# Kernel optimization log

Hardware: AMD Instinct MI355X
Metric: run time of the kernel (lower is better)

Reference implementation:

```python
import jax, jax.numpy as jnp
import numpy as np

T = 2048          # num tokens (prefill)
H = 4096          # hidden_size
NH = 32           # num query heads
NKV = 8           # num kv heads (GQA)
HD = H // NH      # head_dim = 128
BASE = 1000000.0  # rope_theta
NEG = -1e30


def _rope(x, positions):
    # NeoX-style rotary embedding (vLLM default). x: [T, nh, HD]
    half = HD // 2
    inv_freq = 1.0 / (BASE ** (jnp.arange(half, dtype=jnp.float32) / half))
    freqs = positions.astype(jnp.float32)[:, None] * inv_freq  # [T, half]
    cos = jnp.concatenate([jnp.cos(freqs), jnp.cos(freqs)], -1)[:, None, :]
    sin = jnp.concatenate([jnp.sin(freqs), jnp.sin(freqs)], -1)[:, None, :]
    rot = jnp.concatenate([-x[..., half:], x[..., :half]], -1)
    return x * cos + rot * sin


def setup_inputs() -> dict:
    key = jax.random.key(0)
    k1, k2, k3 = jax.random.split(key, 3)
    hidden_states = jax.random.normal(k1, (T, H), jnp.float32)
    wqkv = jax.random.normal(k2, (H, (NH + 2 * NKV) * HD), jnp.float32) * 0.02
    wo = jax.random.normal(k3, (NH * HD, H), jnp.float32) * 0.02
    positions = jnp.arange(T, dtype=jnp.int32)
    return {"positions": positions, "hidden_states": hidden_states,
            "wqkv": wqkv, "wo": wo}


def reference(positions, hidden_states, wqkv, wo):
    # fused QKV projection
    qkv = hidden_states @ wqkv                      # [T, (NH+2*NKV)*HD]
    q, k, v = jnp.split(qkv, [NH * HD, NH * HD + NKV * HD], axis=-1)
    q = q.reshape(T, NH, HD)
    k = k.reshape(T, NKV, HD)
    v = v.reshape(T, NKV, HD)
    # inline RoPE on q, k
    q = _rope(q, positions)
    k = _rope(k, positions)
    # GQA: expand kv heads to query heads
    rep = NH // NKV
    k = jnp.repeat(k, rep, axis=1)                  # [T, NH, HD]
    v = jnp.repeat(v, rep, axis=1)
    # causal scaled dot-product attention (prefill path of PagedAttention)
    scores = jnp.einsum('qhd,khd->hqk', q, k) * (HD ** -0.5)  # [NH, T, T]
    causal = positions[:, None] >= positions[None, :]          # [T, T]
    scores = jnp.where(causal[None, :, :], scores, NEG)
    probs = jax.nn.softmax(scores, axis=-1)
    attn = jnp.einsum('hqk,khd->qhd', probs, v).reshape(T, NH * HD)
    return attn @ wo
```

## Files before the change

### kernel.cpp

```cpp
#include <hip/hip_runtime.h>
#include <hip/hip_bf16.h>

typedef __attribute__((ext_vector_type(8))) short bf16x8;
typedef __attribute__((ext_vector_type(4))) float f32x4;
typedef unsigned short u16;

#define T_TOK 2048
#define HID 4096
#define NH 32
#define NKV 8
#define HD 128
#define QKVN 6144
#define KOFF 4096
#define VOFF 5120

static __device__ __forceinline__ float bf2f(u16 x) {
    union { float f; unsigned u; } v; v.u = ((unsigned)x) << 16; return v.f;
}
static __device__ __forceinline__ u16 f2bf(float f) {
    union { float f; unsigned u; } v; v.f = f;
    unsigned u = v.u;
    unsigned r = (u + 0x7fff + ((u >> 16) & 1)) >> 16;
    return (u16)r;
}

static __device__ __forceinline__ void gload16(const u16* g, u16* l) {
    __builtin_amdgcn_global_load_lds((const __attribute__((address_space(1))) void*)g,
                                     (__attribute__((address_space(3))) void*)l, 16, 0, 0);
}

__global__ __launch_bounds__(256) void convk(const float* __restrict__ in, u16* __restrict__ out) {
    int i = blockIdx.x * 256 + threadIdx.x;
    float4 v = ((const float4*)in)[i];
    ushort4 o;
    o.x = f2bf(v.x); o.y = f2bf(v.y); o.z = f2bf(v.z); o.w = f2bf(v.w);
    ((ushort4*)out)[i] = o;
}

__global__ __launch_bounds__(256) void transpk(const float* __restrict__ in, u16* __restrict__ out,
                                               int R, int C) {
    __shared__ float tile[64][65];
    int c0 = blockIdx.x * 64, r0 = blockIdx.y * 64;
    int tid = threadIdx.x;
#pragma unroll
    for (int it = 0; it < 4; ++it) {
        int ci = it * 256 + tid;
        int r = ci >> 4, c4 = (ci & 15) * 4;
        float4 v = *(const float4*)&in[(size_t)(r0 + r) * C + c0 + c4];
        tile[r][c4 + 0] = v.x; tile[r][c4 + 1] = v.y; tile[r][c4 + 2] = v.z; tile[r][c4 + 3] = v.w;
    }
    __syncthreads();
#pragma unroll
    for (int it = 0; it < 4; ++it) {
        int ci = it * 256 + tid;
        int c = ci >> 4, rq = (ci & 15) * 4;
        ushort4 o;
        o.x = f2bf(tile[rq + 0][c]); o.y = f2bf(tile[rq + 1][c]);
        o.z = f2bf(tile[rq + 2][c]); o.w = f2bf(tile[rq + 3][c]);
        *(ushort4*)&out[(size_t)(c0 + c) * R + r0 + rq] = o;
    }
}

template <int BN, int OUTF32>
__global__ __launch_bounds__(512) void gemm8p(const u16* __restrict__ A, const u16* __restrict__ Bt,
                                              void* __restrict__ Cout, int M, int N, int K) {
    constexpr int BM = 256, BK = 32;
    constexpr int WN = BN / 4;
    constexpr int NF = WN / 16;
    constexpr int ACALLS = 2;
    constexpr int BCALLS = BN / 128;
    constexpr int CALLS = ACALLS + BCALLS;
    constexpr int C1 = 2;
    constexpr int ABUF = BM * BK;
    constexpr int BBUF = BN * BK;
    constexpr int BUFSZ = ABUF + BBUF;

    __shared__ __attribute__((aligned(16))) u16 lds[4 * BUFSZ];

    int bid = blockIdx.x;
    int m0 = (bid & 7) * BM, n0 = (bid >> 3) * BN;
    int tid = threadIdx.x, lane = tid & 63, wid = tid >> 6;
    int wm = wid >> 2, wn = wid & 3;
    int l15 = lane & 15, g4 = lane >> 4;
    int srow = lane >> 2;
    int sslot = (lane & 3) ^ ((lane >> 3) & 3);
    int swz = (g4 ^ ((l15 >> 1) & 3)) * 8;
    int NK = K / BK;

    auto STAGE = [&](int kt, int c) {
        u16* base = &lds[(kt & 3) * BUFSZ];
        size_t kcol = (size_t)kt * BK + sslot * 8;
        if (c < ACALLS) {
            int ch = wid * ACALLS + c;
            gload16(&A[(size_t)(m0 + ch * 16 + srow) * K + kcol], base + ch * 512);
        } else {
            int ch = wid * BCALLS + (c - ACALLS);
            gload16(&Bt[(size_t)(n0 + ch * 16 + srow) * K + kcol], base + ABUF + ch * 512);
        }
    };

    f32x4 acc[8][NF];
#pragma unroll
    for (int i = 0; i < 8; ++i)
#pragma unroll
        for (int j = 0; j < NF; ++j) acc[i][j] = (f32x4){0.f, 0.f, 0.f, 0.f};

    for (int t = 0; t < 3; ++t)
        for (int c = 0; c < CALLS; ++c) STAGE(t, c);
    asm volatile("s_waitcnt vmcnt(%0)" :: "i"(2 * CALLS) : "memory");
    __builtin_amdgcn_s_barrier();
    __builtin_amdgcn_sched_barrier(0);

    for (int g = 0; g < NK; ++g) {
        const u16* ab = &lds[(g & 3) * BUFSZ];
        const u16* bb = ab + ABUF;

        bf16x8 bfr[NF], af[4];
#pragma unroll
        for (int j = 0; j < NF; ++j)
            bfr[j] = *(const bf16x8*)&bb[(wn * WN + j * 16 + l15) * BK + swz];
#pragma unroll
        for (int i = 0; i < 4; ++i)
            af[i] = *(const bf16x8*)&ab[(wm * 128 + i * 16 + l15) * BK + swz];
        if (g + 3 < NK) {
#pragma unroll
            for (int c = 0; c < C1; ++c) STAGE(g + 3, c);
        }
        __builtin_amdgcn_s_setprio(1);
#pragma unroll
        for (int i = 0; i < 4; ++i)
#pragma unroll
            for (int j = 0; j < NF; ++j)
                acc[i][j] = __builtin_amdgcn_mfma_f32_16x16x32_bf16(af[i], bfr[j], acc[i][j], 0, 0, 0);
        __builtin_amdgcn_s_setprio(0);

        bf16x8 af2[4];
#pragma unroll
        for (int i = 0; i < 4; ++i)
            af2[i] = *(const bf16x8*)&ab[(wm * 128 + (4 + i) * 16 + l15) * BK + swz];
        if (g + 3 < NK) {
#pragma unroll
            for (int c = C1; c < CALLS; ++c) STAGE(g + 3, c);
        }
        __builtin_amdgcn_s_setprio(1);
#pragma unroll
        for (int i = 0; i < 4; ++i)
#pragma unroll
            for (int j = 0; j < NF; ++j)
                acc[4 + i][j] = __builtin_amdgcn_mfma_f32_16x16x32_bf16(af2[i], bfr[j], acc[4 + i][j], 0, 0, 0);
        __builtin_amdgcn_s_setprio(0);

        if (g < NK - 3)       asm volatile("s_waitcnt vmcnt(%0)" :: "i"(2 * CALLS) : "memory");
        else if (g == NK - 3) asm volatile("s_waitcnt vmcnt(%0)" :: "i"(CALLS) : "memory");
        else if (g == NK - 2) asm volatile("s_waitcnt vmcnt(0)" ::: "memory");
        __builtin_amdgcn_s_barrier();
        __builtin_amdgcn_sched_barrier(0);
    }

#pragma unroll
    for (int mi = 0; mi < 8; ++mi)
#pragma unroll
        for (int j = 0; j < NF; ++j)
#pragma unroll
            for (int i = 0; i < 4; ++i) {
                int row = m0 + wm * 128 + mi * 16 + g4 * 4 + i;
                int col = n0 + wn * WN + j * 16 + l15;
                float v = acc[mi][j][i];
                if (OUTF32) ((float*)Cout)[(size_t)row * N + col] = v;
                else        ((u16*)Cout)[(size_t)row * N + col] = f2bf(v);
            }
}

__global__ __launch_bounds__(256) void ropek(u16* __restrict__ qkvb, const int* __restrict__ positions) {
    __shared__ float cs_[64], sn_[64];
    int t = blockIdx.x;
    float pos = (float)positions[t];
    if (threadIdx.x < 64) {
        int d = threadIdx.x;
        float inv = exp2f(-(float)d * (19.931568569324174f / 64.0f));
        float fr = pos * inv;
        cs_[d] = cosf(fr);
        sn_[d] = sinf(fr);
    }
    __syncthreads();
#pragma unroll
    for (int it = 0; it < 10; ++it) {
        int ci = it * 256 + threadIdx.x;
        int hh = ci >> 6, d = ci & 63;
        int base = (hh < NH) ? hh * HD : KOFF + (hh - NH) * HD;
        size_t off = (size_t)t * QKVN + base + d;
        float x1 = bf2f(qkvb[off]);
        float x2 = bf2f(qkvb[off + 64]);
        float s = sn_[d], c = cs_[d];
        qkvb[off]      = f2bf(x1 * c - x2 * s);
        qkvb[off + 64] = f2bf(x2 * c + x1 * s);
    }
}

__global__ __launch_bounds__(256) void vtranspk(const u16* __restrict__ qkvb, u16* __restrict__ vT) {
    __shared__ __attribute__((aligned(16))) u16 tile[64][136];
    int kvh = blockIdx.x, t0 = blockIdx.y * 64;
    int tid = threadIdx.x;
#pragma unroll
    for (int it = 0; it < 4; ++it) {
        int ci = it * 256 + tid;
        int r = ci >> 4, c8 = (ci & 15) * 8;
        *(bf16x8*)&tile[r][c8] = *(const bf16x8*)&qkvb[(size_t)(t0 + r) * QKVN + VOFF + kvh * HD + c8];
    }
    __syncthreads();
#pragma unroll
    for (int it = 0; it < 4; ++it) {
        int ci = it * 256 + tid;
        int d = ci >> 3, tc = (ci & 7) * 8;
        union { bf16x8 v; u16 u[8]; } o;
#pragma unroll
        for (int e = 0; e < 8; ++e) o.u[e] = tile[tc + e][d];
        *(bf16x8*)&vT[((size_t)kvh * HD + d) * T_TOK + t0 + tc] = o.v;
    }
}

__global__ __launch_bounds__(256) void attnk(const u16* __restrict__ qkvb, const u16* __restrict__ vT,
                                             u16* __restrict__ attnb) {
    __shared__ __attribute__((aligned(16))) u16 kt_[64 * 136];
    __shared__ __attribute__((aligned(16))) u16 vt_[128 * 72];
    __shared__ __attribute__((aligned(16))) u16 pl_[4 * 16 * 72];
    int h = blockIdx.x, qt = 31 - blockIdx.y;
    int kvh = h >> 2;
    int q0 = qt * 64;
    int tid = threadIdx.x, lane = tid & 63, wid = tid >> 6;
    int l15 = lane & 15, g = lane >> 4;
    const float scale = 0.08838834764831845f;

    int kr = tid >> 4, kc = (tid & 15) * 8;
    int vd = tid >> 3, vc = (tid & 7) * 8;
    const u16* kbase = qkvb + KOFF + (size_t)kvh * HD + kc;
    const u16* vbase = vT + ((size_t)kvh * HD) * T_TOK + vc;

    bf16x8 qf[4];
    int qrow = q0 + wid * 16 + l15;
#pragma unroll
    for (int ks = 0; ks < 4; ++ks)
        qf[ks] = *(const bf16x8*)&qkvb[(size_t)qrow * QKVN + h * HD + ks * 32 + g * 8];

    f32x4 o[8];
#pragma unroll
    for (int df = 0; df < 8; ++df) o[df] = (f32x4){0.f, 0.f, 0.f, 0.f};
    float m_run[4], l_run[4];
#pragma unroll
    for (int i = 0; i < 4; ++i) { m_run[i] = -3.0e38f; l_run[i] = 0.f; }

    bf16x8 kreg[4], vreg[4];
#pragma unroll
    for (int it = 0; it < 4; ++it)
        kreg[it] = *(const bf16x8*)&kbase[(size_t)(it * 16 + kr) * QKVN];
#pragma unroll
    for (int it = 0; it < 4; ++it)
        vreg[it] = *(const bf16x8*)&vbase[(size_t)(it * 32 + vd) * T_TOK];
#pragma unroll
    for (int it = 0; it < 4; ++it) *(bf16x8*)&kt_[(it * 16 + kr) * 136 + kc] = kreg[it];
#pragma unroll
    for (int it = 0; it < 4; ++it) *(bf16x8*)&vt_[(it * 32 + vd) * 72 + vc] = vreg[it];
    {
        int ktl = (1 <= qt) ? 1 : qt;
#pragma unroll
        for (int it = 0; it < 4; ++it)
            kreg[it] = *(const bf16x8*)&kbase[(size_t)(ktl * 64 + it * 16 + kr) * QKVN];
#pragma unroll
        for (int it = 0; it < 4; ++it)
            vreg[it] = *(const bf16x8*)&vbase[(size_t)(it * 32 + vd) * T_TOK + ktl * 64];
    }
    __syncthreads();

    for (int kt2 = 0; kt2 <= qt; ++kt2) {
        int kvb = kt2 * 64;

        f32x4 s[4];
#pragma unroll
        for (int nf = 0; nf < 4; ++nf) s[nf] = (f32x4){0.f, 0.f, 0.f, 0.f};
        __builtin_amdgcn_s_setprio(1);
#pragma unroll
        for (int ks = 0; ks < 4; ++ks) {
#pragma unroll
            for (int nf = 0; nf < 4; ++nf) {
                bf16x8 bfr = *(const bf16x8*)&kt_[(nf * 16 + l15) * 136 + ks * 32 + g * 8];
                s[nf] = __builtin_amdgcn_mfma_f32_16x16x32_bf16(qf[ks], bfr, s[nf], 0, 0, 0);
            }
        }
        __builtin_amdgcn_s_setprio(0);

        float mrow[4];
#pragma unroll
        for (int i = 0; i < 4; ++i) {
            int qr = q0 + wid * 16 + g * 4 + i;
            float mx = -3.0e38f;
#pragma unroll
            for (int nf = 0; nf < 4; ++nf) {
                int kvc = kvb + nf * 16 + l15;
                float v = s[nf][i] * scale;
                v = (kvc <= qr) ? v : -1.0e30f;
                s[nf][i] = v;
                mx = fmaxf(mx, v);
            }
            mrow[i] = mx;
        }
#pragma unroll
        for (int dd = 1; dd < 16; dd <<= 1)
#pragma unroll
            for (int i = 0; i < 4; ++i) mrow[i] = fmaxf(mrow[i], __shfl_xor(mrow[i], dd));

        int ok = 1;
#pragma unroll
        for (int i = 0; i < 4; ++i) ok &= (mrow[i] <= m_run[i] + 8.0f) ? 1 : 0;
        if (!__all(ok)) {
            float alpha[4];
#pragma unroll
            for (int i = 0; i < 4; ++i) {
                float mnew = fmaxf(m_run[i], mrow[i]);
                alpha[i] = __expf(m_run[i] - mnew);
                m_run[i] = mnew;
                l_run[i] *= alpha[i];
            }
#pragma unroll
            for (int df = 0; df < 8; ++df)
#pragma unroll
                for (int i = 0; i < 4; ++i) o[df][i] *= alpha[i];
        }

        float rsum[4] = {0.f, 0.f, 0.f, 0.f};
#pragma unroll
        for (int nf = 0; nf < 4; ++nf)
#pragma unroll
            for (int i = 0; i < 4; ++i) {
                float p = __expf(s[nf][i] - m_run[i]);
                rsum[i] += p;
                pl_[wid * 1152 + (g * 4 + i) * 72 + nf * 16 + l15] = f2bf(p);
            }
#pragma unroll
        for (int dd = 1; dd < 16; dd <<= 1)
#pragma unroll
            for (int i = 0; i < 4; ++i) rsum[i] += __shfl_xor(rsum[i], dd);
#pragma unroll
        for (int i = 0; i < 4; ++i) l_run[i] += rsum[i];

        __builtin_amdgcn_s_setprio(1);
#pragma unroll
        for (int ks2 = 0; ks2 < 2; ++ks2) {
            bf16x8 af = *(const bf16x8*)&pl_[wid * 1152 + l15 * 72 + ks2 * 32 + g * 8];
#pragma unroll
            for (int df = 0; df < 8; ++df) {
                bf16x8 bfr = *(const bf16x8*)&vt_[(df * 16 + l15) * 72 + ks2 * 32 + g * 8];
                o[df] = __builtin_amdgcn_mfma_f32_16x16x32_bf16(af, bfr, o[df], 0, 0, 0);
            }
        }
        __builtin_amdgcn_s_setprio(0);

        if (kt2 < qt) {
            __syncthreads();
#pragma unroll
            for (int it = 0; it < 4; ++it) *(bf16x8*)&kt_[(it * 16 + kr) * 136 + kc] = kreg[it];
#pragma unroll
            for (int it = 0; it < 4; ++it) *(bf16x8*)&vt_[(it * 32 + vd) * 72 + vc] = vreg[it];
            int ktl = (kt2 + 2 <= qt) ? kt2 + 2 : qt;
#pragma unroll
            for (int it = 0; it < 4; ++it)
                kreg[it] = *(const bf16x8*)&kbase[(size_t)(ktl * 64 + it * 16 + kr) * QKVN];
#pragma unroll
            for (int it = 0; it < 4; ++it)
                vreg[it] = *(const bf16x8*)&vbase[(size_t)(it * 32 + vd) * T_TOK + ktl * 64];
            __syncthreads();
        }
    }

#pragma unroll
    for (int df = 0; df < 8; ++df)
#pragma unroll
        for (int i = 0; i < 4; ++i) {
            int qr = q0 + wid * 16 + g * 4 + i;
            int col = h * HD + df * 16 + l15;
            attnb[(size_t)qr * (NH * HD) + col] = f2bf(o[df][i] / l_run[i]);
        }
}

extern "C" void kernel_launch(void* const* d_in, const int* in_sizes, int n_in,
                              void* d_out, int out_size, void* d_ws, size_t ws_size,
                              hipStream_t stream) {
    const int*   positions = (const int*)d_in[0];
    const float* hs        = (const float*)d_in[1];
    const float* wqkv      = (const float*)d_in[2];
    const float* wo        = (const float*)d_in[3];
    float* out = (float*)d_out;

    char* ws = (char*)d_ws;
    u16* hsb   = (u16*)(ws);
    u16* wqkvT = (u16*)(ws + 16777216);
    u16* woT   = (u16*)(ws + 16777216 + 50331648);
    u16* qkvb  = (u16*)(ws + 16777216 + 50331648 + 33554432);
    u16* vT    = (u16*)(ws + 16777216 + 50331648 + 33554432 + 25165824);
    u16* attnb = hsb;

    convk<<<8192, 256, 0, stream>>>(hs, hsb);
    transpk<<<dim3(96, 64), 256, 0, stream>>>(wqkv, wqkvT, HID, QKVN);
    transpk<<<dim3(64, 64), 256, 0, stream>>>(wo, woT, HID, HID);

    gemm8p<256, 0><<<dim3(192), 512, 0, stream>>>(hsb, wqkvT, qkvb, T_TOK, QKVN, HID);

    ropek<<<T_TOK, 256, 0, stream>>>(qkvb, positions);

    vtranspk<<<dim3(NKV, 32), 256, 0, stream>>>(qkvb, vT);

    attnk<<<dim3(NH, 32), 256, 0, stream>>>(qkvb, vT, attnb);

    gemm8p<128, 1><<<dim3(256), 512, 0, stream>>>(attnb, woT, out, T_TOK, HID, HID);
}
```

Baseline: 342.2 us.

## Use 192-wide QKV GEMM tiles, fold attention scale into RoPE, mask only diagonal

The QKV GEMM moves from BN=256 (192 blocks) to BN=192 (256 blocks), so the grid fills the GPU's compute units more evenly. B-tile loads are redistributed across waves, with per-wave vmcnt waits because some waves now issue fewer loads. The softmax scale is folded into Q during the RoPE kernel. The causal mask is applied only on the diagonal KV tile, which removes per-element multiply and compare work from the attention inner loop. Scaling Q before the bf16 rounding slightly changes numerics.

```diff
diff --git a/kernel.cpp b/kernel.cpp
--- a/kernel.cpp
+++ b/kernel.cpp
@@ -13,6 +13,7 @@
 #define QKVN 6144
 #define KOFF 4096
 #define VOFF 5120
+#define ATTN_SCALE 0.08838834764831845f
 
 static __device__ __forceinline__ float bf2f(u16 x) {
     union { float f; unsigned u; } v; v.u = ((unsigned)x) << 16; return v.f;
@@ -28,6 +29,8 @@
     __builtin_amdgcn_global_load_lds((const __attribute__((address_space(1))) void*)g,
                                      (__attribute__((address_space(3))) void*)l, 16, 0, 0);
 }
+
+#define VMC(n) asm volatile("s_waitcnt vmcnt(%0)" :: "i"(n) : "memory")
 
 __global__ __launch_bounds__(256) void convk(const float* __restrict__ in, u16* __restrict__ out) {
     int i = blockIdx.x * 256 + threadIdx.x;
@@ -67,10 +70,9 @@
     constexpr int BM = 256, BK = 32;
     constexpr int WN = BN / 4;
     constexpr int NF = WN / 16;
-    constexpr int ACALLS = 2;
-    constexpr int BCALLS = BN / 128;
-    constexpr int CALLS = ACALLS + BCALLS;
-    constexpr int C1 = 2;
+    constexpr int BCH = BN / 16;
+    constexpr int CA = 2 + (BCH + 7) / 8;
+    constexpr int CB = 2 + BCH / 8;
     constexpr int ABUF = BM * BK;
     constexpr int BBUF = BN * BK;
     constexpr int BUFSZ = ABUF + BBUF;
@@ -86,16 +88,18 @@
     int sslot = (lane & 3) ^ ((lane >> 3) & 3);
     int swz = (g4 ^ ((l15 >> 1) & 3)) * 8;
     int NK = K / BK;
+    bool shortw = (CA != CB) && (wid >= 4);
 
     auto STAGE = [&](int kt, int c) {
         u16* base = &lds[(kt & 3) * BUFSZ];
         size_t kcol = (size_t)kt * BK + sslot * 8;
-        if (c < ACALLS) {
-            int ch = wid * ACALLS + c;
+        if (c < 2) {
+            int ch = wid * 2 + c;
             gload16(&A[(size_t)(m0 + ch * 16 + srow) * K + kcol], base + ch * 512);
         } else {
-            int ch = wid * BCALLS + (c - ACALLS);
-            gload16(&Bt[(size_t)(n0 + ch * 16 + srow) * K + kcol], base + ABUF + ch * 512);
+            int ch = (c - 2) * 8 + wid;
+            if (ch < BCH)
+                gload16(&Bt[(size_t)(n0 + ch * 16 + srow) * K + kcol], base + ABUF + ch * 512);
         }
     };
 
@@ -106,8 +110,8 @@
         for (int j = 0; j < NF; ++j) acc[i][j] = (f32x4){0.f, 0.f, 0.f, 0.f};
 
     for (int t = 0; t < 3; ++t)
-        for (int c = 0; c < CALLS; ++c) STAGE(t, c);
-    asm volatile("s_waitcnt vmcnt(%0)" :: "i"(2 * CALLS) : "memory");
+        for (int c = 0; c < CA; ++c) STAGE(t, c);
+    if (shortw) VMC(2 * CB); else VMC(2 * CA);
     __builtin_amdgcn_s_barrier();
     __builtin_amdgcn_sched_barrier(0);
 
@@ -123,8 +127,7 @@
         for (int i = 0; i < 4; ++i)
             af[i] = *(const bf16x8*)&ab[(wm * 128 + i * 16 + l15) * BK + swz];
         if (g + 3 < NK) {
-#pragma unroll
-            for (int c = 0; c < C1; ++c) STAGE(g + 3, c);
+            STAGE(g + 3, 0); STAGE(g + 3, 1);
         }
         __builtin_amdgcn_s_setprio(1);
 #pragma unroll
@@ -140,7 +143,7 @@
             af2[i] = *(const bf16x8*)&ab[(wm * 128 + (4 + i) * 16 + l15) * BK + swz];
         if (g + 3 < NK) {
 #pragma unroll
-            for (int c = C1; c < CALLS; ++c) STAGE(g + 3, c);
+            for (int c = 2; c < CA; ++c) STAGE(g + 3, c);
         }
         __builtin_amdgcn_s_setprio(1);
 #pragma unroll
@@ -150,9 +153,9 @@
                 acc[4 + i][j] = __builtin_amdgcn_mfma_f32_16x16x32_bf16(af2[i], bfr[j], acc[4 + i][j], 0, 0, 0);
         __builtin_amdgcn_s_setprio(0);
 
-        if (g < NK - 3)       asm volatile("s_waitcnt vmcnt(%0)" :: "i"(2 * CALLS) : "memory");
-        else if (g == NK - 3) asm volatile("s_waitcnt vmcnt(%0)" :: "i"(CALLS) : "memory");
-        else if (g == NK - 2) asm volatile("s_waitcnt vmcnt(0)" ::: "memory");
+        if (g < NK - 3)       { if (shortw) VMC(2 * CB); else VMC(2 * CA); }
+        else if (g == NK - 3) { if (shortw) VMC(CB);     else VMC(CA); }
+        else if (g == NK - 2) VMC(0);
         __builtin_amdgcn_s_barrier();
         __builtin_amdgcn_sched_barrier(0);
     }
@@ -192,8 +195,11 @@
         float x1 = bf2f(qkvb[off]);
         float x2 = bf2f(qkvb[off + 64]);
         float s = sn_[d], c = cs_[d];
-        qkvb[off]      = f2bf(x1 * c - x2 * s);
-        qkvb[off + 64] = f2bf(x2 * c + x1 * s);
+        float y1 = x1 * c - x2 * s;
+        float y2 = x2 * c + x1 * s;
+        if (hh < NH) { y1 *= ATTN_SCALE; y2 *= ATTN_SCALE; }
+        qkvb[off]      = f2bf(y1);
+        qkvb[off + 64] = f2bf(y2);
     }
 }
 
@@ -229,7 +235,6 @@
     int q0 = qt * 64;
     int tid = threadIdx.x, lane = tid & 63, wid = tid >> 6;
     int l15 = lane & 15, g = lane >> 4;
-    const float scale = 0.08838834764831845f;
 
     int kr = tid >> 4, kc = (tid & 15) * 8;
     int vd = tid >> 3, vc = (tid & 7) * 8;
@@ -273,6 +278,7 @@
 
     for (int kt2 = 0; kt2 <= qt; ++kt2) {
         int kvb = kt2 * 64;
+        bool diag = (kt2 == qt);
 
         f32x4 s[4];
 #pragma unroll
@@ -295,10 +301,12 @@
             float mx = -3.0e38f;
 #pragma unroll
             for (int nf = 0; nf < 4; ++nf) {
-                int kvc = kvb + nf * 16 + l15;
-                float v = s[nf][i] * scale;
-                v = (kvc <= qr) ? v : -1.0e30f;
-                s[nf][i] = v;
+                float v = s[nf][i];
+                if (diag) {
+                    int kvc = kvb + nf * 16 + l15;
+                    v = (kvc <= qr) ? v : -1.0e30f;
+                    s[nf][i] = v;
+                }
                 mx = fmaxf(mx, v);
             }
             mrow[i] = mx;
@@ -402,7 +410,7 @@
     transpk<<<dim3(96, 64), 256, 0, stream>>>(wqkv, wqkvT, HID, QKVN);
     transpk<<<dim3(64, 64), 256, 0, stream>>>(wo, woT, HID, HID);
 
-    gemm8p<256, 0><<<dim3(192), 512, 0, stream>>>(hsb, wqkvT, qkvb, T_TOK, QKVN, HID);
+    gemm8p<192, 0><<<dim3(256), 512, 0, stream>>>(hsb, wqkvT, qkvb, T_TOK, QKVN, HID);
 
     ropek<<<T_TOK, 256, 0, stream>>>(qkvb, positions);
 
```

New measurement: 339.6 us. No clear change (-0.8%).
